# Performance work log

Measured on AMD Instinct MI355X. Metric: run time of the kernel, lower is better.

Reference implementation:

```python
import jax, jax.numpy as jnp
import numpy as np

N = 100_000      # nodes
E = 1_600_000    # edges (before self loops)
IN = 128         # in_dim
HID = 64         # hidden_dim (per head)
HEADS = 2
NEG_SLOPE = 0.2  # PyG GATConv default negative_slope


def setup_inputs() -> dict:
    key = jax.random.key(0)
    k = jax.random.split(key, 6)
    x = jax.random.normal(k[0], (N, IN), jnp.float32)
    edge_index = jax.random.randint(k[1], (2, E), 0, N, dtype=jnp.int64)
    # GATConv linear (no bias in lin, bias added after aggregation in PyG)
    W = jax.random.normal(k[2], (IN, HEADS * HID), jnp.float32) * (1.0 / np.sqrt(IN))
    att_src = jax.random.normal(k[3], (HEADS, HID), jnp.float32) * 0.1
    att_dst = jax.random.normal(k[4], (HEADS, HID), jnp.float32) * 0.1
    bias = jnp.zeros((HEADS * HID,), jnp.float32)
    prelu_w = jnp.full((HEADS * HID,), 0.25, jnp.float32)  # nn.PReLU default init
    return {"x": x, "edge_index": edge_index, "W": W, "att_src": att_src,
            "att_dst": att_dst, "bias": bias, "prelu_w": prelu_w}


def reference(x, edge_index, W, att_src, att_dst, bias, prelu_w):
    n = x.shape[0]
    h = (x @ W).reshape(n, HEADS, HID)                 # [N,H,C]
    a_s = jnp.einsum('nhc,hc->nh', h, att_src)         # [N,H]
    a_d = jnp.einsum('nhc,hc->nh', h, att_dst)         # [N,H]
    # add self loops (PyG default add_self_loops=True)
    loops = jnp.arange(n, dtype=edge_index.dtype)
    src = jnp.concatenate([edge_index[0], loops])      # [Et]
    dst = jnp.concatenate([edge_index[1], loops])      # [Et]
    logits = a_s[src] + a_d[dst]                       # [Et,H]
    logits = jnp.where(logits >= 0, logits, NEG_SLOPE * logits)  # LeakyReLU
    # segment softmax over destination neighborhoods
    m = jax.ops.segment_max(logits, dst, num_segments=n)         # [N,H]
    e = jnp.exp(logits - m[dst])
    s = jax.ops.segment_sum(e, dst, num_segments=n)              # [N,H]
    alpha = e / (s[dst] + 1e-16)                                 # [Et,H]
    # (attention dropout p=0.2 is identity in eval mode)
    msg = h[src] * alpha[..., None]                    # [Et,H,C]
    out = jax.ops.segment_sum(msg, dst, num_segments=n).reshape(n, HEADS * HID)
    out = out + bias
    # PReLU with per-channel weight
    return jnp.where(out >= 0, out, prelu_w * out)
```

## Files before the change

kernel.cpp:

```cpp
#include <hip/hip_runtime.h>
#include <hip/hip_fp16.h>
#include <cstdint>
#include <cstddef>

#define NEG_SLOPE 0.2f
#define BSH 9
#define BNODES 512
#define CAP 12288

typedef __attribute__((ext_vector_type(8))) short short8v;
typedef __attribute__((ext_vector_type(4))) float f32x4;

__device__ __forceinline__ uint32_t bf16pair(float a, float b) {
    uint32_t ua = __float_as_uint(a), ub = __float_as_uint(b);
    ua = (ua + 0x7fffu + ((ua >> 16) & 1u)) >> 16;
    ub = (ub + 0x7fffu + ((ub >> 16) & 1u)) >> 16;
    return ua | (ub << 16);
}
__device__ __forceinline__ uint16_t rne16(float f) {
    uint32_t u = __float_as_uint(f);
    return (uint16_t)((u + 0x7fffu + ((u >> 16) & 1u)) >> 16);
}
__device__ __forceinline__ float bflo(uint32_t u) { return __uint_as_float(u << 16); }
__device__ __forceinline__ float bfhi(uint32_t u) { return __uint_as_float(u & 0xffff0000u); }
__device__ __forceinline__ uint32_t packf16(float a, float b) {
    __half2 h = __floats2half2_rn(a, b);
    return *reinterpret_cast<uint32_t*>(&h);
}

__global__ __launch_bounds__(256, 3) void gemm_att(
    const float* __restrict__ x, const float* __restrict__ W,
    const float* __restrict__ att_src, const float* __restrict__ att_dst,
    uint32_t* __restrict__ hb, float* __restrict__ a_s, float* __restrict__ a_d,
    int* __restrict__ gcur, int nb, int n)
{
    constexpr int PW = 136;
    __shared__ unsigned short Wt[128 * PW];
    __shared__ unsigned short Hs[4][16 * PW];
    const int tid  = threadIdx.x;
    const int w    = tid >> 6;
    const int lane = tid & 63;
    const int cl   = lane & 15;
    const int gq   = lane >> 4;
    const int base = blockIdx.x * 64;

    if (blockIdx.x == 0 && tid < nb) gcur[tid] = 0;

    const float4* W4 = (const float4*)W;
#pragma unroll
    for (int i = 0; i < 16; ++i) {
        int idx = tid + i * 256;
        int k = idx >> 5, c0 = (idx & 31) * 4;
        float4 v = W4[idx];
        Wt[(c0 + 0) * PW + k] = rne16(v.x);
        Wt[(c0 + 1) * PW + k] = rne16(v.y);
        Wt[(c0 + 2) * PW + k] = rne16(v.z);
        Wt[(c0 + 3) * PW + k] = rne16(v.w);
    }

    float asr[8], adr[8];
#pragma unroll
    for (int t = 0; t < 8; ++t) {
        asr[t] = att_src[t * 16 + cl];
        adr[t] = att_dst[t * 16 + cl];
    }
    __syncthreads();

    const int rowg = base + w * 16 + cl;
    const int rowc = rowg < n ? rowg : (n - 1);
    const float4* xp = (const float4*)(x + (size_t)rowc * 128);

    f32x4 acc[8];
#pragma unroll
    for (int t = 0; t < 8; ++t) acc[t] = (f32x4){0.f, 0.f, 0.f, 0.f};

#pragma unroll
    for (int s = 0; s < 4; ++s) {
        int kq = s * 8 + gq * 2;
        float4 f0 = xp[kq], f1 = xp[kq + 1];
        union { short8v v; uint32_t d[4]; } A;
        A.d[0] = bf16pair(f0.x, f0.y);
        A.d[1] = bf16pair(f0.z, f0.w);
        A.d[2] = bf16pair(f1.x, f1.y);
        A.d[3] = bf16pair(f1.z, f1.w);
#pragma unroll
        for (int t = 0; t < 8; ++t) {
            union { short8v v; uint4 q; } B;
            B.q = *(const uint4*)&Wt[(t * 16 + cl) * PW + s * 32 + gq * 8];
            acc[t] = __builtin_amdgcn_mfma_f32_16x16x32_bf16(A.v, B.v, acc[t], 0, 0, 0);
        }
    }

    float ps0[4], ps1[4], pd0[4], pd1[4];
#pragma unroll
    for (int r = 0; r < 4; ++r) { ps0[r] = ps1[r] = pd0[r] = pd1[r] = 0.f; }
#pragma unroll
    for (int t = 0; t < 8; ++t) {
#pragma unroll
        for (int r = 0; r < 4; ++r) {
            float v = acc[t][r];
            if (t < 4) { ps0[r] = fmaf(v, asr[t], ps0[r]); pd0[r] = fmaf(v, adr[t], pd0[r]); }
            else       { ps1[r] = fmaf(v, asr[t], ps1[r]); pd1[r] = fmaf(v, adr[t], pd1[r]); }
        }
    }
#pragma unroll
    for (int off = 1; off < 16; off <<= 1) {
#pragma unroll
        for (int r = 0; r < 4; ++r) {
            ps0[r] += __shfl_xor(ps0[r], off);
            ps1[r] += __shfl_xor(ps1[r], off);
            pd0[r] += __shfl_xor(pd0[r], off);
            pd1[r] += __shfl_xor(pd1[r], off);
        }
    }
    if (cl == 0) {
#pragma unroll
        for (int r = 0; r < 4; ++r) {
            int rg = base + w * 16 + gq * 4 + r;
            if (rg < n) {
                a_s[rg * 2 + 0] = ps0[r]; a_s[rg * 2 + 1] = ps1[r];
                a_d[rg * 2 + 0] = pd0[r]; a_d[rg * 2 + 1] = pd1[r];
            }
        }
    }

#pragma unroll
    for (int t = 0; t < 8; ++t) {
#pragma unroll
        for (int r = 0; r < 4; ++r) {
            int row = gq * 4 + r;
            Hs[w][row * PW + t * 16 + cl] = rne16(acc[t][r]);
        }
    }
    __syncthreads();
#pragma unroll
    for (int q = 0; q < 4; ++q) {
        int row = q * 4 + gq;
        int cu  = 4 * cl;
        uint4 v = *(const uint4*)&Hs[w][row * PW + cu * 2];
        int rg = base + w * 16 + row;
        if (rg < n) *(uint4*)&hb[(size_t)rg * 64 + cu] = v;
    }
}

__global__ __launch_bounds__(256) void bucket_scatter(
    const int* __restrict__ src, const int* __restrict__ dst,
    int* __restrict__ gcur, uint32_t* __restrict__ pairs, int e, int nb)
{
    __shared__ int histL[256];
    __shared__ int gbaseL[256];
    const int tid = threadIdx.x;
    const int t0  = blockIdx.x * 4096;

    if (tid < nb) histL[tid] = 0;
    __syncthreads();

    int      myb[16];
    int      myslot[16];
    uint32_t mypk[16];
#pragma unroll 16
    for (int k = 0; k < 16; ++k) {
        int i = t0 + tid + k * 256;
        if (i < e) {
            int s = src[i], d = dst[i];
            int b = d >> BSH;
            myb[k]    = b;
            mypk[k]   = (uint32_t)s | ((uint32_t)(d & (BNODES - 1)) << 17);
            myslot[k] = atomicAdd(&histL[b], 1);
        } else myb[k] = -1;
    }
    __syncthreads();
    if (tid < nb) {
        int c = histL[tid];
        gbaseL[tid] = c ? atomicAdd(&gcur[tid], c) : 0;
    }
    __syncthreads();
#pragma unroll 16
    for (int k = 0; k < 16; ++k) {
        if (myb[k] >= 0) {
            int p = gbaseL[myb[k]] + myslot[k];
            if (p < CAP) pairs[(size_t)myb[k] * CAP + p] = mypk[k];
        }
    }
}

__global__ __launch_bounds__(512, 2) void build_csr(
    const uint32_t* __restrict__ pairs, const int* __restrict__ gcur,
    const float* __restrict__ a_s, const float* __restrict__ a_d,
    uint4* __restrict__ meta, uint2* __restrict__ edges, int n, int nb)
{
    __shared__ uint32_t pl[CAP];
    __shared__ int degL[BNODES], curL[BNODES];
    __shared__ float sumL[BNODES * 2];
    __shared__ float adL[BNODES * 2];
    __shared__ int bscan[256];
    __shared__ int wsum[8];
    const int b = blockIdx.x, tid = threadIdx.x;
    const int lane = tid & 63, wid = tid >> 6;
    const int nbase = b * BNODES;
    const int nodes = min(BNODES, n - nbase);

    if (tid < 256) {
        int tot = 0;
        if (tid < nb) {
            int nn = min(BNODES, n - tid * BNODES);
            tot = min(gcur[tid], CAP) + nn;
        }
        bscan[tid] = tot;
    }
    __syncthreads();
    for (int off = 1; off < 256; off <<= 1) {
        int t = 0;
        if (tid < 256 && tid >= off) t = bscan[tid - off];
        __syncthreads();
        if (tid < 256) bscan[tid] += t;
        __syncthreads();
    }
    const int C    = min(gcur[b], CAP);
    const int base = bscan[b] - (C + nodes);

    degL[tid] = 1;
    float es0 = 0.f, es1 = 0.f;
    if (tid < nodes) {
        int g = nbase + tid;
        float2 ad = ((const float2*)a_d)[g];
        adL[2 * tid]     = ad.x;
        adL[2 * tid + 1] = ad.y;
        float2 as = ((const float2*)a_s)[g];
        float l0 = as.x + ad.x; l0 = l0 >= 0.f ? l0 : NEG_SLOPE * l0;
        float l1 = as.y + ad.y; l1 = l1 >= 0.f ? l1 : NEG_SLOPE * l1;
        es0 = __expf(l0); es1 = __expf(l1);
        sumL[2 * tid] = es0; sumL[2 * tid + 1] = es1;
    }
    __syncthreads();
    for (int i = tid; i < C; i += 512) {
        uint32_t p = pairs[(size_t)b * CAP + i];
        pl[i] = p;
        atomicAdd(&degL[p >> 17], 1);
    }
    __syncthreads();

    int v = (tid < nodes) ? degL[tid] : 0;
    int sc = v;
#pragma unroll
    for (int off = 1; off < 64; off <<= 1) {
        int t = __shfl_up(sc, off);
        if (lane >= off) sc += t;
    }
    if (lane == 63) wsum[wid] = sc;
    __syncthreads();
    int woff = 0;
#pragma unroll
    for (int k = 0; k < 8; ++k) woff += (k < wid) ? wsum[k] : 0;
    const int exc = sc - v + woff;

    if (tid < nodes) {
        edges[base + exc] = make_uint2((uint32_t)(nbase + tid), packf16(es0, es1));
        curL[tid] = exc + 1;
    }
    __syncthreads();
    for (int i = tid; i < C; i += 512) {
        uint32_t p  = pl[i];
        int dl  = p >> 17;
        int s   = p & 0x1FFFF;
        float2 as = ((const float2*)a_s)[s];
        float l0 = as.x + adL[2 * dl];     l0 = l0 >= 0.f ? l0 : NEG_SLOPE * l0;
        float l1 = as.y + adL[2 * dl + 1]; l1 = l1 >= 0.f ? l1 : NEG_SLOPE * l1;
        float e0 = __expf(l0), e1 = __expf(l1);
        int pos = atomicAdd(&curL[dl], 1);
        edges[base + pos] = make_uint2((uint32_t)s, packf16(e0, e1));
        atomicAdd(&sumL[2 * dl],     e0);
        atomicAdd(&sumL[2 * dl + 1], e1);
    }
    __syncthreads();
    if (tid < nodes) {
        uint4 m;
        m.x = (uint32_t)(base + exc);
        m.y = (uint32_t)v;
        m.z = __float_as_uint(1.f / (sumL[2 * tid]     + 1e-16f));
        m.w = __float_as_uint(1.f / (sumL[2 * tid + 1] + 1e-16f));
        meta[nbase + tid] = m;
    }
}

__global__ __launch_bounds__(256) void attn_agg(
    const uint32_t* __restrict__ hb, const uint2* __restrict__ edges,
    const uint4* __restrict__ meta,
    const float* __restrict__ bias, const float* __restrict__ prelu_w,
    float* __restrict__ out, int n)
{
    const int gw   = (blockIdx.x * blockDim.x + threadIdx.x) >> 6;
    const int lane = threadIdx.x & 63;
    if (gw >= n) return;
    const uint4 mt  = meta[gw];
    const int start = (int)mt.x;
    const int deg   = (int)mt.y;
    const float inv0 = __uint_as_float(mt.z);
    const float inv1 = __uint_as_float(mt.w);

    if (deg <= 64) {
        int sv = 0; float al0 = 0.f, al1 = 0.f;
        if (lane < deg) {
            uint2 ed = edges[start + lane];
            sv = (int)ed.x;
            __half2 h2 = *reinterpret_cast<__half2*>(&ed.y);
            al0 = __half2float(__low2half(h2))  * inv0;
            al1 = __half2float(__high2half(h2)) * inv1;
        }
        const int g = lane >> 4, r = lane & 15;
        float acc[8];
#pragma unroll
        for (int q = 0; q < 8; ++q) acc[q] = 0.f;

        const uint4* hb4 = (const uint4*)hb;
        const int iters = (deg + 7) >> 3;
        for (int jj = 0; jj < iters; ++jj) {
            const int ja = jj * 8 + g, jb = ja + 4;
            int   sa  = __shfl(sv, ja);
            int   sb  = __shfl(sv, jb);
            float A0a = __shfl(al0, ja), A1a = __shfl(al1, ja);
            float A0b = __shfl(al0, jb), A1b = __shfl(al1, jb);
            float Aa  = (r < 8) ? A0a : A1a;
            float Ab  = (r < 8) ? A0b : A1b;
            uint4 qa = hb4[(size_t)sa * 16 + r];
            uint4 qb = hb4[(size_t)sb * 16 + r];
            acc[0] = fmaf(Aa, bflo(qa.x), acc[0]);
            acc[1] = fmaf(Aa, bfhi(qa.x), acc[1]);
            acc[2] = fmaf(Aa, bflo(qa.y), acc[2]);
            acc[3] = fmaf(Aa, bfhi(qa.y), acc[3]);
            acc[4] = fmaf(Aa, bflo(qa.z), acc[4]);
            acc[5] = fmaf(Aa, bfhi(qa.z), acc[5]);
            acc[6] = fmaf(Aa, bflo(qa.w), acc[6]);
            acc[7] = fmaf(Aa, bfhi(qa.w), acc[7]);
            acc[0] = fmaf(Ab, bflo(qb.x), acc[0]);
            acc[1] = fmaf(Ab, bfhi(qb.x), acc[1]);
            acc[2] = fmaf(Ab, bflo(qb.y), acc[2]);
            acc[3] = fmaf(Ab, bfhi(qb.y), acc[3]);
            acc[4] = fmaf(Ab, bflo(qb.z), acc[4]);
            acc[5] = fmaf(Ab, bfhi(qb.z), acc[5]);
            acc[6] = fmaf(Ab, bflo(qb.w), acc[6]);
            acc[7] = fmaf(Ab, bfhi(qb.w), acc[7]);
        }
#pragma unroll
        for (int q = 0; q < 8; ++q) {
            acc[q] += __shfl_xor(acc[q], 16);
            acc[q] += __shfl_xor(acc[q], 32);
        }
        if (lane < 16) {
            float4 b0 = ((const float4*)bias)[lane * 2];
            float4 b1 = ((const float4*)bias)[lane * 2 + 1];
            float4 p0 = ((const float4*)prelu_w)[lane * 2];
            float4 p1 = ((const float4*)prelu_w)[lane * 2 + 1];
            float4 w0, w1;
            w0.x = acc[0] + b0.x; w0.x = w0.x >= 0.f ? w0.x : p0.x * w0.x;
            w0.y = acc[1] + b0.y; w0.y = w0.y >= 0.f ? w0.y : p0.y * w0.y;
            w0.z = acc[2] + b0.z; w0.z = w0.z >= 0.f ? w0.z : p0.z * w0.z;
            w0.w = acc[3] + b0.w; w0.w = w0.w >= 0.f ? w0.w : p0.w * w0.w;
            w1.x = acc[4] + b1.x; w1.x = w1.x >= 0.f ? w1.x : p1.x * w1.x;
            w1.y = acc[5] + b1.y; w1.y = w1.y >= 0.f ? w1.y : p1.y * w1.y;
            w1.z = acc[6] + b1.z; w1.z = w1.z >= 0.f ? w1.z : p1.z * w1.z;
            w1.w = acc[7] + b1.w; w1.w = w1.w >= 0.f ? w1.w : p1.w * w1.w;
            ((float4*)out)[(size_t)gw * 32 + lane * 2]     = w0;
            ((float4*)out)[(size_t)gw * 32 + lane * 2 + 1] = w1;
        }
    } else {
        float accL = 0.f, accH = 0.f;
        for (int t0 = 0; t0 < deg; t0 += 64) {
            int tt = t0 + lane;
            int sv = 0; float al0 = 0.f, al1 = 0.f;
            if (tt < deg) {
                uint2 ed = edges[start + tt];
                sv = (int)ed.x;
                __half2 h2 = *reinterpret_cast<__half2*>(&ed.y);
                al0 = __half2float(__low2half(h2))  * inv0;
                al1 = __half2float(__high2half(h2)) * inv1;
            }
            int kmax = min(64, deg - t0);
            for (int j = 0; j < kmax; ++j) {
                int   s  = __shfl(sv, j);
                float A0 = __shfl(al0, j);
                float A1 = __shfl(al1, j);
                float A  = (lane < 32) ? A0 : A1;
                uint32_t u = hb[(size_t)s * 64 + lane];
                accL = fmaf(A, bflo(u), accL);
                accH = fmaf(A, bfhi(u), accH);
            }
        }
        float2 bz = ((const float2*)bias)[lane];
        float2 pw = ((const float2*)prelu_w)[lane];
        float o0 = accL + bz.x, o1 = accH + bz.y;
        o0 = o0 >= 0.f ? o0 : pw.x * o0;
        o1 = o1 >= 0.f ? o1 : pw.y * o1;
        float2 rr; rr.x = o0; rr.y = o1;
        ((float2*)out)[(size_t)gw * 64 + lane] = rr;
    }
}

extern "C" void kernel_launch(void* const* d_in, const int* in_sizes, int n_in,
                              void* d_out, int out_size, void* d_ws, size_t ws_size,
                              hipStream_t stream)
{
    const float* x        = (const float*)d_in[0];
    const int*   ei       = (const int*)d_in[1];
    const float* W        = (const float*)d_in[2];
    const float* att_src  = (const float*)d_in[3];
    const float* att_dst  = (const float*)d_in[4];
    const float* bias     = (const float*)d_in[5];
    const float* prelu_w  = (const float*)d_in[6];
    float* out = (float*)d_out;

    const int n = in_sizes[0] / 128;
    const int e = in_sizes[1] / 2;
    const int* srcp = ei;
    const int* dstp = ei + e;
    const int nb = (n + BNODES - 1) / BNODES;

    uint32_t* hb    = (uint32_t*)d_ws;
    uint4*    meta  = (uint4*)(hb + (size_t)n * 64);
    float*    a_s   = (float*)(meta + n);
    float*    a_d   = a_s + (size_t)n * 2;
    int*      gcur  = (int*)(a_d + (size_t)n * 2);
    uint32_t* pairs = (uint32_t*)(gcur + 256);
    uint2*    edges = (uint2*)(pairs + (size_t)nb * CAP);

    gemm_att<<<(n + 63) / 64, 256, 0, stream>>>(x, W, att_src, att_dst,
                                                hb, a_s, a_d, gcur, nb, n);
    bucket_scatter<<<(e + 4095) / 4096, 256, 0, stream>>>(srcp, dstp, gcur, pairs, e, nb);
    build_csr<<<nb, 512, 0, stream>>>(pairs, gcur, a_s, a_d, meta, edges, n, nb);
    attn_agg<<<(n + 3) / 4, 256, 0, stream>>>(hb, edges, meta, bias, prelu_w, out, n);
}
```

Before: 158.9 us.

## Shrink CSR buckets, add nontemporal loads/stores, and unroll gather by four

Halves the destination bucket size (256 nodes, smaller capacity), so twice as many build_csr blocks run with less LDS each. The bucket prefix scan is rewritten as a wave-shuffle scan to handle up to 512 buckets. Nontemporal loads and stores are applied to streaming data such as x, edge lists, pairs and the output. The short-degree aggregation loop now gathers four neighbor rows per iteration instead of two to raise memory-level parallelism. The lower per-bucket capacity (about 20 average edges per node) leaves less headroom for skewed degree distributions, and edges beyond it would be silently dropped.

```diff
diff --git a/kernel.cpp b/kernel.cpp
--- a/kernel.cpp
+++ b/kernel.cpp
@@ -4,12 +4,13 @@
 #include <cstddef>
 
 #define NEG_SLOPE 0.2f
-#define BSH 9
-#define BNODES 512
-#define CAP 12288
+#define BSH 8
+#define BNODES 256
+#define CAP 5120
 
 typedef __attribute__((ext_vector_type(8))) short short8v;
 typedef __attribute__((ext_vector_type(4))) float f32x4;
+typedef __attribute__((ext_vector_type(2))) uint32_t u32x2;
 
 __device__ __forceinline__ uint32_t bf16pair(float a, float b) {
     uint32_t ua = __float_as_uint(a), ub = __float_as_uint(b);
@@ -44,7 +45,8 @@
     const int gq   = lane >> 4;
     const int base = blockIdx.x * 64;
 
-    if (blockIdx.x == 0 && tid < nb) gcur[tid] = 0;
+    if (blockIdx.x == 0)
+        for (int i = tid; i < nb; i += 256) gcur[i] = 0;
 
     const float4* W4 = (const float4*)W;
 #pragma unroll
@@ -68,7 +70,7 @@
 
     const int rowg = base + w * 16 + cl;
     const int rowc = rowg < n ? rowg : (n - 1);
-    const float4* xp = (const float4*)(x + (size_t)rowc * 128);
+    const f32x4* xp = (const f32x4*)(x + (size_t)rowc * 128);
 
     f32x4 acc[8];
 #pragma unroll
@@ -77,7 +79,8 @@
 #pragma unroll
     for (int s = 0; s < 4; ++s) {
         int kq = s * 8 + gq * 2;
-        float4 f0 = xp[kq], f1 = xp[kq + 1];
+        f32x4 f0 = __builtin_nontemporal_load(xp + kq);
+        f32x4 f1 = __builtin_nontemporal_load(xp + kq + 1);
         union { short8v v; uint32_t d[4]; } A;
         A.d[0] = bf16pair(f0.x, f0.y);
         A.d[1] = bf16pair(f0.z, f0.w);
@@ -147,12 +150,12 @@
     const int* __restrict__ src, const int* __restrict__ dst,
     int* __restrict__ gcur, uint32_t* __restrict__ pairs, int e, int nb)
 {
-    __shared__ int histL[256];
-    __shared__ int gbaseL[256];
+    __shared__ int histL[512];
+    __shared__ int gbaseL[512];
     const int tid = threadIdx.x;
     const int t0  = blockIdx.x * 4096;
 
-    if (tid < nb) histL[tid] = 0;
+    for (int i = tid; i < nb; i += 256) histL[i] = 0;
     __syncthreads();
 
     int      myb[16];
@@ -162,7 +165,8 @@
     for (int k = 0; k < 16; ++k) {
         int i = t0 + tid + k * 256;
         if (i < e) {
-            int s = src[i], d = dst[i];
+            int s = __builtin_nontemporal_load(src + i);
+            int d = __builtin_nontemporal_load(dst + i);
             int b = d >> BSH;
             myb[k]    = b;
             mypk[k]   = (uint32_t)s | ((uint32_t)(d & (BNODES - 1)) << 17);
@@ -170,9 +174,9 @@
         } else myb[k] = -1;
     }
     __syncthreads();
-    if (tid < nb) {
-        int c = histL[tid];
-        gbaseL[tid] = c ? atomicAdd(&gcur[tid], c) : 0;
+    for (int i = tid; i < nb; i += 256) {
+        int c = histL[i];
+        gbaseL[i] = c ? atomicAdd(&gcur[i], c) : 0;
     }
     __syncthreads();
 #pragma unroll 16
@@ -184,7 +188,7 @@
     }
 }
 
-__global__ __launch_bounds__(512, 2) void build_csr(
+__global__ __launch_bounds__(512) void build_csr(
     const uint32_t* __restrict__ pairs, const int* __restrict__ gcur,
     const float* __restrict__ a_s, const float* __restrict__ a_d,
     uint4* __restrict__ meta, uint2* __restrict__ edges, int n, int nb)
@@ -193,33 +197,33 @@
     __shared__ int degL[BNODES], curL[BNODES];
     __shared__ float sumL[BNODES * 2];
     __shared__ float adL[BNODES * 2];
-    __shared__ int bscan[256];
-    __shared__ int wsum[8];
+    __shared__ int bscan[512];
+    __shared__ int wsum8[8];
     const int b = blockIdx.x, tid = threadIdx.x;
     const int lane = tid & 63, wid = tid >> 6;
     const int nbase = b * BNODES;
     const int nodes = min(BNODES, n - nbase);
 
-    if (tid < 256) {
-        int tot = 0;
-        if (tid < nb) {
-            int nn = min(BNODES, n - tid * BNODES);
-            tot = min(gcur[tid], CAP) + nn;
-        }
-        bscan[tid] = tot;
-    }
-    __syncthreads();
-    for (int off = 1; off < 256; off <<= 1) {
-        int t = 0;
-        if (tid < 256 && tid >= off) t = bscan[tid - off];
-        __syncthreads();
-        if (tid < 256) bscan[tid] += t;
-        __syncthreads();
-    }
-    const int C    = min(gcur[b], CAP);
-    const int base = bscan[b] - (C + nodes);
-
-    degL[tid] = 1;
+    int tot = 0;
+    if (tid < nb) {
+        int nn = min(BNODES, n - tid * BNODES);
+        tot = min(gcur[tid], CAP) + nn;
+    }
+    int sc = tot;
+#pragma unroll
+    for (int off = 1; off < 64; off <<= 1) {
+        int t = __shfl_up(sc, off);
+        if (lane >= off) sc += t;
+    }
+    if (lane == 63) wsum8[wid] = sc;
+    __syncthreads();
+    {
+        int woff = 0;
+#pragma unroll
+        for (int k = 0; k < 8; ++k) woff += (k < wid) ? wsum8[k] : 0;
+        bscan[tid] = sc + woff;
+    }
+    if (tid < BNODES) degL[tid] = 1;
     float es0 = 0.f, es1 = 0.f;
     if (tid < nodes) {
         int g = nbase + tid;
@@ -233,26 +237,29 @@
         sumL[2 * tid] = es0; sumL[2 * tid + 1] = es1;
     }
     __syncthreads();
+    const int C    = min(gcur[b], CAP);
+    const int base = bscan[b] - (C + nodes);
+
     for (int i = tid; i < C; i += 512) {
-        uint32_t p = pairs[(size_t)b * CAP + i];
+        uint32_t p = __builtin_nontemporal_load(pairs + (size_t)b * CAP + i);
         pl[i] = p;
         atomicAdd(&degL[p >> 17], 1);
     }
     __syncthreads();
 
     int v = (tid < nodes) ? degL[tid] : 0;
-    int sc = v;
+    int sc2 = v;
 #pragma unroll
     for (int off = 1; off < 64; off <<= 1) {
-        int t = __shfl_up(sc, off);
-        if (lane >= off) sc += t;
-    }
-    if (lane == 63) wsum[wid] = sc;
-    __syncthreads();
-    int woff = 0;
-#pragma unroll
-    for (int k = 0; k < 8; ++k) woff += (k < wid) ? wsum[k] : 0;
-    const int exc = sc - v + woff;
+        int t = __shfl_up(sc2, off);
+        if (lane >= off) sc2 += t;
+    }
+    if (lane == 63 && tid < BNODES) wsum8[wid] = sc2;
+    __syncthreads();
+    int woff2 = 0;
+#pragma unroll
+    for (int k = 0; k < 4; ++k) woff2 += (k < wid) ? wsum8[k] : 0;
+    const int exc = sc2 - v + woff2;
 
     if (tid < nodes) {
         edges[base + exc] = make_uint2((uint32_t)(nbase + tid), packf16(es0, es1));
@@ -301,9 +308,10 @@
     if (deg <= 64) {
         int sv = 0; float al0 = 0.f, al1 = 0.f;
         if (lane < deg) {
-            uint2 ed = edges[start + lane];
+            u32x2 ed = __builtin_nontemporal_load((const u32x2*)(edges + start + lane));
             sv = (int)ed.x;
-            __half2 h2 = *reinterpret_cast<__half2*>(&ed.y);
+            uint32_t ey = ed.y;
+            __half2 h2 = *reinterpret_cast<__half2*>(&ey);
             al0 = __half2float(__low2half(h2))  * inv0;
             al1 = __half2float(__high2half(h2)) * inv1;
         }
@@ -313,33 +321,41 @@
         for (int q = 0; q < 8; ++q) acc[q] = 0.f;
 
         const uint4* hb4 = (const uint4*)hb;
-        const int iters = (deg + 7) >> 3;
+        const int iters = (deg + 15) >> 4;
         for (int jj = 0; jj < iters; ++jj) {
-            const int ja = jj * 8 + g, jb = ja + 4;
-            int   sa  = __shfl(sv, ja);
-            int   sb  = __shfl(sv, jb);
-            float A0a = __shfl(al0, ja), A1a = __shfl(al1, ja);
-            float A0b = __shfl(al0, jb), A1b = __shfl(al1, jb);
-            float Aa  = (r < 8) ? A0a : A1a;
-            float Ab  = (r < 8) ? A0b : A1b;
-            uint4 qa = hb4[(size_t)sa * 16 + r];
-            uint4 qb = hb4[(size_t)sb * 16 + r];
-            acc[0] = fmaf(Aa, bflo(qa.x), acc[0]);
-            acc[1] = fmaf(Aa, bfhi(qa.x), acc[1]);
-            acc[2] = fmaf(Aa, bflo(qa.y), acc[2]);
-            acc[3] = fmaf(Aa, bfhi(qa.y), acc[3]);
-            acc[4] = fmaf(Aa, bflo(qa.z), acc[4]);
-            acc[5] = fmaf(Aa, bfhi(qa.z), acc[5]);
-            acc[6] = fmaf(Aa, bflo(qa.w), acc[6]);
-            acc[7] = fmaf(Aa, bfhi(qa.w), acc[7]);
-            acc[0] = fmaf(Ab, bflo(qb.x), acc[0]);
-            acc[1] = fmaf(Ab, bfhi(qb.x), acc[1]);
-            acc[2] = fmaf(Ab, bflo(qb.y), acc[2]);
-            acc[3] = fmaf(Ab, bfhi(qb.y), acc[3]);
-            acc[4] = fmaf(Ab, bflo(qb.z), acc[4]);
-            acc[5] = fmaf(Ab, bfhi(qb.z), acc[5]);
-            acc[6] = fmaf(Ab, bflo(qb.w), acc[6]);
-            acc[7] = fmaf(Ab, bfhi(qb.w), acc[7]);
+            const int j0 = jj * 16 + g;
+            int   s0  = __shfl(sv, j0);
+            int   s1  = __shfl(sv, j0 + 4);
+            int   s2  = __shfl(sv, j0 + 8);
+            int   s3  = __shfl(sv, j0 + 12);
+            float A00 = __shfl(al0, j0),      A10 = __shfl(al1, j0);
+            float A01 = __shfl(al0, j0 + 4),  A11 = __shfl(al1, j0 + 4);
+            float A02 = __shfl(al0, j0 + 8),  A12 = __shfl(al1, j0 + 8);
+            float A03 = __shfl(al0, j0 + 12), A13 = __shfl(al1, j0 + 12);
+            float Aa = (r < 8) ? A00 : A10;
+            float Ab = (r < 8) ? A01 : A11;
+            float Ac = (r < 8) ? A02 : A12;
+            float Ad = (r < 8) ? A03 : A13;
+            uint4 qa = hb4[(size_t)s0 * 16 + r];
+            uint4 qb = hb4[(size_t)s1 * 16 + r];
+            uint4 qc = hb4[(size_t)s2 * 16 + r];
+            uint4 qd = hb4[(size_t)s3 * 16 + r];
+            acc[0] = fmaf(Aa, bflo(qa.x), acc[0]); acc[1] = fmaf(Aa, bfhi(qa.x), acc[1]);
+            acc[2] = fmaf(Aa, bflo(qa.y), acc[2]); acc[3] = fmaf(Aa, bfhi(qa.y), acc[3]);
+            acc[4] = fmaf(Aa, bflo(qa.z), acc[4]); acc[5] = fmaf(Aa, bfhi(qa.z), acc[5]);
+            acc[6] = fmaf(Aa, bflo(qa.w), acc[6]); acc[7] = fmaf(Aa, bfhi(qa.w), acc[7]);
+            acc[0] = fmaf(Ab, bflo(qb.x), acc[0]); acc[1] = fmaf(Ab, bfhi(qb.x), acc[1]);
+            acc[2] = fmaf(Ab, bflo(qb.y), acc[2]); acc[3] = fmaf(Ab, bfhi(qb.y), acc[3]);
+            acc[4] = fmaf(Ab, bflo(qb.z), acc[4]); acc[5] = fmaf(Ab, bfhi(qb.z), acc[5]);
+            acc[6] = fmaf(Ab, bflo(qb.w), acc[6]); acc[7] = fmaf(Ab, bfhi(qb.w), acc[7]);
+            acc[0] = fmaf(Ac, bflo(qc.x), acc[0]); acc[1] = fmaf(Ac, bfhi(qc.x), acc[1]);
+            acc[2] = fmaf(Ac, bflo(qc.y), acc[2]); acc[3] = fmaf(Ac, bfhi(qc.y), acc[3]);
+            acc[4] = fmaf(Ac, bflo(qc.z), acc[4]); acc[5] = fmaf(Ac, bfhi(qc.z), acc[5]);
+            acc[6] = fmaf(Ac, bflo(qc.w), acc[6]); acc[7] = fmaf(Ac, bfhi(qc.w), acc[7]);
+            acc[0] = fmaf(Ad, bflo(qd.x), acc[0]); acc[1] = fmaf(Ad, bfhi(qd.x), acc[1]);
+            acc[2] = fmaf(Ad, bflo(qd.y), acc[2]); acc[3] = fmaf(Ad, bfhi(qd.y), acc[3]);
+            acc[4] = fmaf(Ad, bflo(qd.z), acc[4]); acc[5] = fmaf(Ad, bfhi(qd.z), acc[5]);
+            acc[6] = fmaf(Ad, bflo(qd.w), acc[6]); acc[7] = fmaf(Ad, bfhi(qd.w), acc[7]);
         }
 #pragma unroll
         for (int q = 0; q < 8; ++q) {
@@ -351,7 +367,7 @@
             float4 b1 = ((const float4*)bias)[lane * 2 + 1];
             float4 p0 = ((const float4*)prelu_w)[lane * 2];
             float4 p1 = ((const float4*)prelu_w)[lane * 2 + 1];
-            float4 w0, w1;
+            f32x4 w0, w1;
             w0.x = acc[0] + b0.x; w0.x = w0.x >= 0.f ? w0.x : p0.x * w0.x;
             w0.y = acc[1] + b0.y; w0.y = w0.y >= 0.f ? w0.y : p0.y * w0.y;
             w0.z = acc[2] + b0.z; w0.z = w0.z >= 0.f ? w0.z : p0.z * w0.z;
@@ -360,8 +376,9 @@
             w1.y = acc[5] + b1.y; w1.y = w1.y >= 0.f ? w1.y : p1.y * w1.y;
             w1.z = acc[6] + b1.z; w1.z = w1.z >= 0.f ? w1.z : p1.z * w1.z;
             w1.w = acc[7] + b1.w; w1.w = w1.w >= 0.f ? w1.w : p1.w * w1.w;
-            ((float4*)out)[(size_t)gw * 32 + lane * 2]     = w0;
-            ((float4*)out)[(size_t)gw * 32 + lane * 2 + 1] = w1;
+            float* op = out + (size_t)gw * 128 + lane * 8;
+            __builtin_nontemporal_store(w0, (f32x4*)op);
+            __builtin_nontemporal_store(w1, (f32x4*)(op + 4));
         }
     } else {
         float accL = 0.f, accH = 0.f;
@@ -420,7 +437,7 @@
     float*    a_s   = (float*)(meta + n);
     float*    a_d   = a_s + (size_t)n * 2;
     int*      gcur  = (int*)(a_d + (size_t)n * 2);
-    uint32_t* pairs = (uint32_t*)(gcur + 256);
+    uint32_t* pairs = (uint32_t*)(gcur + 512);
     uint2*    edges = (uint2*)(pairs + (size_t)nb * CAP);
 
     gemm_att<<<(n + 63) / 64, 256, 0, stream>>>(x, W, att_src, att_dst,
```

New measurement: 160.5 us. Within noise of the previous version (+1.0%).
